# Optimization experiments

Hardware: AMD Instinct MI355X
Metric: run time of the kernel (lower is better)

Reference implementation:

```python
import jax, jax.numpy as jnp
import numpy as np

GROUP_SIZE = 16
E2M1_MAX = 6.0
# Positive E2M1 grid and midpoints for round-to-nearest
E2M1_POS = jnp.array([0.0, 0.5, 1.0, 1.5, 2.0, 3.0, 4.0, 6.0], jnp.float32)
E2M1_MID = jnp.array([0.25, 0.75, 1.25, 1.75, 2.5, 3.5, 5.0], jnp.float32)
# Full 16-entry signed LUT (bit3 = sign, sign-magnitude)
E2M1_LUT = jnp.array([0.0, 0.5, 1.0, 1.5, 2.0, 3.0, 4.0, 6.0,
                      -0.0, -0.5, -1.0, -1.5, -2.0, -3.0, -4.0, -6.0], jnp.float32)

def _round_e2m1(x):
    # nearest value on the E2M1 grid (clamped to +-6)
    idx = jnp.searchsorted(E2M1_MID, jnp.abs(x))
    return jnp.sign(x) * E2M1_POS[idx]

def nvfp4_act_qdq(x, input_scale):
    # per-group dynamic quantize to NVFP4 with fp8-e4m3 group scale, then dequantize
    orig_shape = x.shape
    xg = x.astype(jnp.float32).reshape(*orig_shape[:-1], -1, GROUP_SIZE)
    amax = jnp.max(jnp.abs(xg), axis=-1, keepdims=True)
    s = (amax / (E2M1_MAX * input_scale)).astype(jnp.float8_e4m3fn).astype(jnp.float32)
    s = jnp.where(s > 0, s, 1.0)
    total = s * input_scale  # effective per-group scale
    dq = _round_e2m1(xg / total) * total
    return dq.reshape(orig_shape).astype(jnp.float16)

def nvfp4_dequantize(weight, weight_scale, weight_scale_2):
    # weight: [O, I//2] packed bytes (values 0..255); low nibble = even index
    O = weight.shape[0]
    low = weight & 0xF
    high = (weight >> 4) & 0xF
    codes = jnp.stack([low, high], axis=-1).reshape(O, -1)  # [O, I]
    vals = E2M1_LUT[codes].reshape(O, -1, GROUP_SIZE)       # [O, G, 16]
    w = vals * weight_scale[:, :, None] * weight_scale_2
    return w.reshape(O, -1).astype(jnp.float16)

def setup_inputs() -> dict:
    key = jax.random.key(0)
    k1, k2, k3 = jax.random.split(key, 3)
    B, S, I, O = 8, 16, 8192, 8192
    hidden_states = jax.random.normal(k1, (B, S, I), dtype=jnp.float16)
    weight = jax.random.randint(k2, (O, I // 2), 0, 256, dtype=jnp.int32)
    weight_scale = jax.random.uniform(k3, (O, I // GROUP_SIZE), dtype=jnp.float32) * 0.05 + 0.001
    weight_scale_2 = jnp.ones((1,), jnp.float32)
    input_scale = jnp.ones((1,), jnp.float32)
    return {"hidden_states": hidden_states, "weight": weight,
            "weight_scale": weight_scale, "weight_scale_2": weight_scale_2,
            "input_scale": input_scale}

def reference(hidden_states, weight, weight_scale, weight_scale_2, input_scale):
    hs_dq = nvfp4_act_qdq(hidden_states, input_scale)
    w_dq = nvfp4_dequantize(weight, weight_scale, weight_scale_2)
    return jnp.matmul(hs_dq, w_dq.T)  # [B, S, O], fp16
```

## Files before the change

### kernel.cpp

```cpp
#include <hip/hip_runtime.h>
#include <stdint.h>


typedef _Float16 half8 __attribute__((ext_vector_type(8)));
typedef float float4v __attribute__((ext_vector_type(4)));

__device__ __forceinline__ uint32_t perm_b32(uint32_t hi, uint32_t lo, uint32_t sel) {
  return __builtin_amdgcn_perm(hi, lo, sel);
}

__device__ __forceinline__ float e4m3_roundtrip(float x) {
  if (x < 0.015625f) {
    return __builtin_rintf(x * 512.0f) * 0.001953125f;
  }
  uint32_t u = __float_as_uint(x);
  u += 0x7FFFFu + ((u >> 20) & 1u);
  u &= 0xFFF00000u;
  float y = __uint_as_float(u);
  return fminf(y, 448.0f);
}

__global__ __launch_bounds__(256)
void aqdq_kernel(const float* __restrict__ hs,
                 const float* __restrict__ isc,
                 uint4* __restrict__ asw) {
  const int t = blockIdx.x * 256 + threadIdx.x;
  const int m = t >> 9;
  const int g = t & 511;
  const float* p = hs + m * 8192 + g * 16;
  float x[16];
#pragma unroll
  for (int q = 0; q < 4; ++q) *(float4*)&x[q * 4] = ((const float4*)p)[q];
  float amax = 0.0f;
#pragma unroll
  for (int i = 0; i < 16; ++i) amax = fmaxf(amax, fabsf(x[i]));

  float is = isc[0];
  float s = e4m3_roundtrip(amax / (6.0f * is));
  if (!(s > 0.0f)) s = 1.0f;
  float total = s * is;

  union { _Float16 h[16]; uint4 v4[2]; } qq;
#pragma unroll
  for (int i = 0; i < 16; ++i) {
    float r = x[i] / total;
    float a = fabsf(r);
    float v = (a <= 0.25f) ? 0.0f
            : (a <= 0.75f) ? 0.5f
            : (a <= 1.25f) ? 1.0f
            : (a <= 1.75f) ? 1.5f
            : (a <= 2.5f)  ? 2.0f
            : (a <= 3.5f)  ? 3.0f
            : (a <= 5.0f)  ? 4.0f : 6.0f;
    qq.h[i] = (_Float16)(copysignf(v, r) * total);
  }
  const int mb = m >> 4;
#pragma unroll
  for (int hf = 0; hf < 2; ++hf) {
    int k = g * 16 + hf * 8;
    int kb = k >> 5;
    int quad = (k >> 3) & 3;
    int lane = (m & 15) | (quad << 4);
    asw[(kb * 8 + mb) * 64 + lane] = qq.v4[hf];
  }
}

__device__ __forceinline__ half8 decode_scale(int4 w, float sf) {
  uint32_t t0 = perm_b32((uint32_t)w.y, (uint32_t)w.x, 0x00000400u);
  uint32_t t1 = perm_b32((uint32_t)w.w, (uint32_t)w.z, 0x04000000u);
  uint32_t b  = perm_b32(t1, t0, 0x07060100u);
  uint32_t ev = b & 0x0F0F0F0Fu;
  uint32_t od = (b >> 4) & 0x0F0F0F0Fu;
  uint32_t evm = ev & 0x07070707u;
  uint32_t odm = od & 0x07070707u;
  uint32_t evs = (ev & 0x08080808u) << 4;
  uint32_t ods = (od & 0x08080808u) << 4;
  uint32_t evh = perm_b32(0x46444240u, 0x3E3C3800u, evm) | evs;
  uint32_t odh = perm_b32(0x46444240u, 0x3E3C3800u, odm) | ods;
  union { uint32_t u[4]; half8 h; } r;
  r.u[0] = perm_b32(odh, evh, 0x04000000u) & 0xFF00FF00u;
  r.u[1] = perm_b32(odh, evh, 0x05000100u) & 0xFF00FF00u;
  r.u[2] = perm_b32(odh, evh, 0x06000200u) & 0xFF00FF00u;
  r.u[3] = perm_b32(odh, evh, 0x07000300u) & 0xFF00FF00u;
  _Float16 hsf = (_Float16)sf;
  half8 sv = {hsf, hsf, hsf, hsf, hsf, hsf, hsf, hsf};
  return r.h * sv;
}

__global__ __launch_bounds__(512)
void gemm_kernel(const uint4* __restrict__ asw,
                 const int* __restrict__ wq,
                 const float* __restrict__ wsc,
                 const float* __restrict__ ws2p,
                 float* __restrict__ out) {
  __shared__ float red[8][32][136];
  const int lane = threadIdx.x & 63;
  const int wv = threadIdx.x >> 6;
  const int quad = lane >> 4;
  const int n0 = blockIdx.x * 32;
  const int rA = n0 + (lane & 15);
  const int rB = rA + 16;
  const float ws2 = ws2p[0];
  const int4* wpA = (const int4*)(wq + rA * 4096);
  const int4* wpB = (const int4*)(wq + rB * 4096);
  const float* wsA = wsc + rA * 512;
  const float* wsB = wsc + rB * 512;
  const int kbase = wv * 1024;

  float4v acc[2][8];
#pragma unroll
  for (int ng = 0; ng < 2; ++ng)
#pragma unroll
    for (int mb = 0; mb < 8; ++mb) acc[ng][mb] = (float4v){0.f, 0.f, 0.f, 0.f};

  const uint4* ap = asw + (kbase >> 5) * 512 + lane;

#pragma unroll 2
  for (int ks = 0; ks < 32; ++ks) {
    const int k0 = kbase + ks * 32;
    const int wi = (k0 >> 3) + quad;
    int4 wA = wpA[wi];
    int4 wB = wpB[wi];
    const int si = (k0 >> 4) + (quad >> 1);
    float sA = wsA[si] * ws2;
    float sB = wsB[si] * ws2;
    uint4 af[8];
#pragma unroll
    for (int mb = 0; mb < 8; ++mb) af[mb] = ap[ks * 512 + mb * 64];
    half8 bA = decode_scale(wA, sA);
    half8 bB = decode_scale(wB, sB);
#pragma unroll
    for (int mb = 0; mb < 8; ++mb) {
      union { uint4 u; half8 h; } a;
      a.u = af[mb];
      acc[0][mb] = __builtin_amdgcn_mfma_f32_16x16x32_f16(a.h, bA, acc[0][mb], 0, 0, 0);
      acc[1][mb] = __builtin_amdgcn_mfma_f32_16x16x32_f16(a.h, bB, acc[1][mb], 0, 0, 0);
    }
  }

#pragma unroll
  for (int ng = 0; ng < 2; ++ng)
#pragma unroll
    for (int mb = 0; mb < 8; ++mb) {
      *(float4v*)&red[wv][ng * 16 + (lane & 15)][mb * 16 + quad * 4] = acc[ng][mb];
    }
  __syncthreads();

  const int t = threadIdx.x;
  const int m = t >> 2;
  const int ng8 = (t & 3) * 8;
  float o[8];
#pragma unroll
  for (int j = 0; j < 8; ++j) {
    float s = 0.f;
#pragma unroll
    for (int p = 0; p < 8; ++p) s += red[p][ng8 + j][m];
    o[j] = s;
  }
  float* op = out + m * 8192 + n0 + ng8;
  *(float4*)&op[0] = *(float4*)&o[0];
  *(float4*)&op[4] = *(float4*)&o[4];
}

extern "C" void kernel_launch(void* const* d_in, const int* in_sizes, int n_in,
                              void* d_out, int out_size, void* d_ws, size_t ws_size,
                              hipStream_t stream) {
  (void)in_sizes; (void)n_in; (void)out_size; (void)ws_size;
  const float* hs  = (const float*)d_in[0];
  const int* wq    = (const int*)d_in[1];
  const float* wsc = (const float*)d_in[2];
  const float* ws2 = (const float*)d_in[3];
  const float* isc = (const float*)d_in[4];
  float* out       = (float*)d_out;
  uint4* asw       = (uint4*)d_ws;

  aqdq_kernel<<<256, 256, 0, stream>>>(hs, isc, asw);
  gemm_kernel<<<256, 512, 0, stream>>>(asw, wq, wsc, ws2, out);
}
```

Before: 253.3 us.

## Halve GEMM N-tile per block and split activation quantization across four threads

The GEMM block now covers 16 output columns instead of 32, doubling the grid to 512 blocks and shrinking accumulators and the shared reduction buffer so more blocks can be resident. The goal is better occupancy and latency hiding across the CUs. The cost is that each activation fragment is reloaded twice as often across blocks. The activation quantize kernel now uses four threads per 16-element group, with shuffles for the group max and 8-byte stores, to spread the work over more threads.

```diff
diff --git a/kernel.cpp b/kernel.cpp
--- a/kernel.cpp
+++ b/kernel.cpp
@@ -23,27 +23,30 @@
 __global__ __launch_bounds__(256)
 void aqdq_kernel(const float* __restrict__ hs,
                  const float* __restrict__ isc,
-                 uint4* __restrict__ asw) {
+                 uint2* __restrict__ asw) {
   const int t = blockIdx.x * 256 + threadIdx.x;
-  const int m = t >> 9;
-  const int g = t & 511;
-  const float* p = hs + m * 8192 + g * 16;
-  float x[16];
-#pragma unroll
-  for (int q = 0; q < 4; ++q) *(float4*)&x[q * 4] = ((const float4*)p)[q];
-  float amax = 0.0f;
-#pragma unroll
-  for (int i = 0; i < 16; ++i) amax = fmaxf(amax, fabsf(x[i]));
+  const int m = t >> 11;
+  const int u = t & 2047;
+  const int g = u >> 2;
+  const int hq = u & 3;
+
+  const float* p = hs + m * 8192 + g * 16 + hq * 4;
+  float4 x = *(const float4*)p;
+
+  float amax = fmaxf(fmaxf(fabsf(x.x), fabsf(x.y)), fmaxf(fabsf(x.z), fabsf(x.w)));
+  amax = fmaxf(amax, __shfl_xor(amax, 1));
+  amax = fmaxf(amax, __shfl_xor(amax, 2));
 
   float is = isc[0];
   float s = e4m3_roundtrip(amax / (6.0f * is));
   if (!(s > 0.0f)) s = 1.0f;
   float total = s * is;
 
-  union { _Float16 h[16]; uint4 v4[2]; } qq;
+  float xv[4] = {x.x, x.y, x.z, x.w};
+  union { _Float16 h[4]; uint2 v; } qq;
 #pragma unroll
-  for (int i = 0; i < 16; ++i) {
-    float r = x[i] / total;
+  for (int i = 0; i < 4; ++i) {
+    float r = xv[i] / total;
     float a = fabsf(r);
     float v = (a <= 0.25f) ? 0.0f
             : (a <= 0.75f) ? 0.5f
@@ -54,15 +57,13 @@
             : (a <= 5.0f)  ? 4.0f : 6.0f;
     qq.h[i] = (_Float16)(copysignf(v, r) * total);
   }
+
+  const int k = g * 16 + hq * 4;
+  const int kb = k >> 5;
+  const int quad = (k >> 3) & 3;
+  const int lane16 = (m & 15) | (quad << 4);
   const int mb = m >> 4;
-#pragma unroll
-  for (int hf = 0; hf < 2; ++hf) {
-    int k = g * 16 + hf * 8;
-    int kb = k >> 5;
-    int quad = (k >> 3) & 3;
-    int lane = (m & 15) | (quad << 4);
-    asw[(kb * 8 + mb) * 64 + lane] = qq.v4[hf];
-  }
+  asw[((kb * 8 + mb) * 64 + lane16) * 2 + (hq & 1)] = qq.v;
 }
 
 __device__ __forceinline__ half8 decode_scale(int4 w, float sf) {
@@ -87,79 +88,65 @@
   return r.h * sv;
 }
 
-__global__ __launch_bounds__(512)
+__global__ __launch_bounds__(512, 4)
 void gemm_kernel(const uint4* __restrict__ asw,
                  const int* __restrict__ wq,
                  const float* __restrict__ wsc,
                  const float* __restrict__ ws2p,
                  float* __restrict__ out) {
-  __shared__ float red[8][32][136];
+  __shared__ float red[8][16][132];
   const int lane = threadIdx.x & 63;
   const int wv = threadIdx.x >> 6;
   const int quad = lane >> 4;
-  const int n0 = blockIdx.x * 32;
+  const int n0 = blockIdx.x * 16;
   const int rA = n0 + (lane & 15);
-  const int rB = rA + 16;
   const float ws2 = ws2p[0];
   const int4* wpA = (const int4*)(wq + rA * 4096);
-  const int4* wpB = (const int4*)(wq + rB * 4096);
   const float* wsA = wsc + rA * 512;
-  const float* wsB = wsc + rB * 512;
   const int kbase = wv * 1024;
 
-  float4v acc[2][8];
+  float4v acc[8];
 #pragma unroll
-  for (int ng = 0; ng < 2; ++ng)
-#pragma unroll
-    for (int mb = 0; mb < 8; ++mb) acc[ng][mb] = (float4v){0.f, 0.f, 0.f, 0.f};
+  for (int mb = 0; mb < 8; ++mb) acc[mb] = (float4v){0.f, 0.f, 0.f, 0.f};
 
   const uint4* ap = asw + (kbase >> 5) * 512 + lane;
 
 #pragma unroll 2
   for (int ks = 0; ks < 32; ++ks) {
     const int k0 = kbase + ks * 32;
-    const int wi = (k0 >> 3) + quad;
-    int4 wA = wpA[wi];
-    int4 wB = wpB[wi];
-    const int si = (k0 >> 4) + (quad >> 1);
-    float sA = wsA[si] * ws2;
-    float sB = wsB[si] * ws2;
+    int4 wA = wpA[(k0 >> 3) + quad];
+    float2 sv = *(const float2*)(wsA + (k0 >> 4));
+    float sA = ((quad & 2) ? sv.y : sv.x) * ws2;
     uint4 af[8];
 #pragma unroll
     for (int mb = 0; mb < 8; ++mb) af[mb] = ap[ks * 512 + mb * 64];
     half8 bA = decode_scale(wA, sA);
-    half8 bB = decode_scale(wB, sB);
 #pragma unroll
     for (int mb = 0; mb < 8; ++mb) {
       union { uint4 u; half8 h; } a;
       a.u = af[mb];
-      acc[0][mb] = __builtin_amdgcn_mfma_f32_16x16x32_f16(a.h, bA, acc[0][mb], 0, 0, 0);
-      acc[1][mb] = __builtin_amdgcn_mfma_f32_16x16x32_f16(a.h, bB, acc[1][mb], 0, 0, 0);
+      acc[mb] = __builtin_amdgcn_mfma_f32_16x16x32_f16(a.h, bA, acc[mb], 0, 0, 0);
     }
   }
 
 #pragma unroll
-  for (int ng = 0; ng < 2; ++ng)
-#pragma unroll
-    for (int mb = 0; mb < 8; ++mb) {
-      *(float4v*)&red[wv][ng * 16 + (lane & 15)][mb * 16 + quad * 4] = acc[ng][mb];
-    }
+  for (int mb = 0; mb < 8; ++mb) {
+    *(float4v*)&red[wv][lane & 15][mb * 16 + quad * 4] = acc[mb];
+  }
   __syncthreads();
 
   const int t = threadIdx.x;
   const int m = t >> 2;
-  const int ng8 = (t & 3) * 8;
-  float o[8];
+  const int j0 = (t & 3) * 4;
+  float o[4];
 #pragma unroll
-  for (int j = 0; j < 8; ++j) {
+  for (int j = 0; j < 4; ++j) {
     float s = 0.f;
 #pragma unroll
-    for (int p = 0; p < 8; ++p) s += red[p][ng8 + j][m];
+    for (int p = 0; p < 8; ++p) s += red[p][j0 + j][m];
     o[j] = s;
   }
-  float* op = out + m * 8192 + n0 + ng8;
-  *(float4*)&op[0] = *(float4*)&o[0];
-  *(float4*)&op[4] = *(float4*)&o[4];
+  *(float4*)&out[m * 8192 + n0 + j0] = *(float4*)&o[0];
 }
 
 extern "C" void kernel_launch(void* const* d_in, const int* in_sizes, int n_in,
@@ -172,8 +159,9 @@
   const float* ws2 = (const float*)d_in[3];
   const float* isc = (const float*)d_in[4];
   float* out       = (float*)d_out;
-  uint4* asw       = (uint4*)d_ws;
+  uint2* asw2      = (uint2*)d_ws;
+  const uint4* asw4 = (const uint4*)d_ws;
 
-  aqdq_kernel<<<256, 256, 0, stream>>>(hs, isc, asw);
-  gemm_kernel<<<256, 512, 0, stream>>>(asw, wq, wsc, ws2, out);
+  aqdq_kernel<<<1024, 256, 0, stream>>>(hs, isc, asw2);
+  gemm_kernel<<<512, 512, 0, stream>>>(asw4, wq, wsc, ws2, out);
 }
```

Measured after the change: 265.4 us. 1.05x slower.
